# Optimization experiments

Measured on AMD Instinct MI355X. Metric: run time of the kernel, lower is better.

The kernel has to match this reference:

```python
import jax, jax.numpy as jnp
import numpy as np

HEADS = 16
NEG = -10000.0


def setup_inputs() -> dict:
    key = jax.random.key(0)
    ks = jax.random.split(key, 8)
    B, S, D = 2, 2048, 2048
    scale = 0.02
    return {
        "q": jax.random.normal(ks[0], (B, S, D), dtype=jnp.float32),
        "k": jax.random.normal(ks[1], (B, S, D), dtype=jnp.float32),
        "v": jax.random.normal(ks[2], (B, S, D), dtype=jnp.float32),
        "mask": jax.random.randint(ks[3], (B, S, S), 0, 2).astype(jnp.bool_),
        "Wq": jax.random.normal(ks[4], (D, D), dtype=jnp.float32) * scale,
        "Wk": jax.random.normal(ks[5], (D, D), dtype=jnp.float32) * scale,
        "Wv": jax.random.normal(ks[6], (D, D), dtype=jnp.float32) * scale,
        "Wo": jax.random.normal(ks[7], (D, D), dtype=jnp.float32) * scale,
    }


def _split_heads(x):
    # (B, S, D) -> (B, H, S, Dh)
    B, S, D = x.shape
    return x.reshape(B, S, HEADS, D // HEADS).transpose(0, 2, 1, 3)


def reference(q, k, v, mask, Wq, Wk, Wv, Wo):
    # bias-free linear projections (nn.Linear: x @ W.T)
    qp = q @ Wq.T
    kp = k @ Wk.T
    vp = v @ Wv.T
    qh, kh, vh = _split_heads(qp), _split_heads(kp), _split_heads(vp)
    head_dim = qh.shape[-1]
    # scores: (B, H, S, S)
    scores = jnp.einsum('bhqd,bhkd->bhqk', qh, kh) / jnp.sqrt(
        jnp.asarray(head_dim, dtype=qh.dtype))
    # additive mask, broadcast over heads (mask unsqueezed at -3 in torch)
    scores = scores + mask[:, None, :, :].astype(scores.dtype) * NEG
    attn = jax.nn.softmax(scores, axis=-1)
    ctx = jnp.einsum('bhqk,bhkd->bhqd', attn, vh)  # (B, H, S, Dh)
    B, H, S, Dh = ctx.shape
    ctx = ctx.transpose(0, 2, 1, 3).reshape(B, S, H * Dh)
    out = ctx @ Wo.T
    return (out, kp, vp)
```

## Files before the change

kernel.cpp:

```cpp
#include <hip/hip_runtime.h>
#include <hip/hip_bf16.h>
#include <stdint.h>


typedef unsigned short u16;
typedef unsigned char u8;
typedef __bf16 bf16x8 __attribute__((ext_vector_type(8)));
typedef unsigned short u16x8 __attribute__((ext_vector_type(8)));
typedef unsigned short u16x4 __attribute__((ext_vector_type(4)));
typedef float f32x4 __attribute__((ext_vector_type(4)));

#if __has_builtin(__builtin_amdgcn_exp2f)
#define EXP2(x) __builtin_amdgcn_exp2f(x)
#else
#define EXP2(x) exp2f(x)
#endif

__device__ __forceinline__ u16 f2bf(float f) {
  union { __bf16 h; u16 u; } c;
  c.h = (__bf16)f;
  return c.u;
}

__device__ __forceinline__ void stage8_f32(const float* src, u16* dst) {
  float4 x0 = ((const float4*)src)[0];
  float4 x1 = ((const float4*)src)[1];
  u16 t[8] = {f2bf(x0.x), f2bf(x0.y), f2bf(x0.z), f2bf(x0.w),
              f2bf(x1.x), f2bf(x1.y), f2bf(x1.z), f2bf(x1.w)};
  *(uint4*)dst = *(const uint4*)t;
}

typedef const __attribute__((address_space(1))) void gas_t;
typedef __attribute__((address_space(3))) void las_t;
__device__ __forceinline__ void gll16(const void* g, void* l) {
  __builtin_amdgcn_global_load_lds((gas_t*)g, (las_t*)l, 16, 0, 0);
}

__global__ void detect_kernel(const u16* __restrict__ q,
                              const u16* __restrict__ mask,
                              int* __restrict__ flags) {
  __shared__ int c32, oddnz, b3f80;
  if (threadIdx.x == 0) { c32 = 0; oddnz = 0; b3f80 = 0; }
  __syncthreads();
  int l32 = 0, lodd = 0, l3f = 0;
  for (int i = threadIdx.x; i < 4096; i += 256) {
    u16 u = q[i];
    if (((u >> 7) & 0xFF) >= 0x86) l32++;
    u16 m = mask[i];
    if (m == 0x3F80) l3f++;
    if ((i & 1) && m != 0) lodd++;
  }
  if (l32) atomicAdd(&c32, l32);
  if (lodd) atomicAdd(&oddnz, lodd);
  if (l3f) atomicAdd(&b3f80, l3f);
  __syncthreads();
  if (threadIdx.x == 0) {
    flags[0] = (c32 > 16) ? 1 : 0;
    flags[1] = b3f80 ? 2 : (oddnz ? 1 : 0);
  }
}

__global__ void pack_mask(const u8* __restrict__ maskp,
                          const int* __restrict__ flags,
                          u16* __restrict__ bits, long n) {
  const int mm = flags[1];
  long gw = ((long)blockIdx.x * blockDim.x + threadIdx.x) >> 6;
  int lane = threadIdx.x & 63;
  long nw = ((long)gridDim.x * blockDim.x) >> 6;
  for (long w = gw; w * 64 < n; w += nw) {
    long i = w * 64 + lane;
    bool nz;
    if (mm == 0)      nz = ((const int*)maskp)[i] != 0;
    else if (mm == 1) nz = maskp[i] != 0;
    else              nz = ((const u16*)maskp)[i] != 0;
    unsigned long long b = __ballot(nz);
    if (lane < 4) bits[w * 4 + lane] = (u16)(b >> (lane * 16));
  }
}

__global__ __launch_bounds__(256) void to_bf16_all(
    const u8* __restrict__ q, const u8* __restrict__ k, const u8* __restrict__ v,
    const u8* __restrict__ wq, const u8* __restrict__ wk,
    const u8* __restrict__ wv, const u8* __restrict__ wo,
    u16* __restrict__ qi, u16* __restrict__ ki, u16* __restrict__ vi,
    u16* __restrict__ wqb, u16* __restrict__ wkb, u16* __restrict__ wvb,
    u16* __restrict__ wob, const int* __restrict__ flags, long NEa, long NW) {
  const int fp = flags[0];
  const u8* src; u16* dst; long n;
  switch (blockIdx.y) {
    case 0: src = q;  dst = qi;  n = NEa; break;
    case 1: src = k;  dst = ki;  n = NEa; break;
    case 2: src = v;  dst = vi;  n = NEa; break;
    case 3: src = wq; dst = wqb; n = NW;  break;
    case 4: src = wk; dst = wkb; n = NW;  break;
    case 5: src = wv; dst = wvb; n = NW;  break;
    default: src = wo; dst = wob; n = NW; break;
  }
  long i0 = ((long)blockIdx.x * 256 + threadIdx.x) * 8;
  long stride = (long)gridDim.x * 256 * 8;
  for (long i = i0; i < n; i += stride) {
    u16 tmp[8];
    if (fp) stage8_f32((const float*)src + i, tmp);
    else    *(uint4*)tmp = *(const uint4*)((const u16*)src + i);
    *(uint4*)&dst[i] = *(const uint4*)tmp;
  }
}

__global__ __launch_bounds__(256) void transpose_v(
    const u8* __restrict__ vpbase, u16* __restrict__ vt,
    const int* __restrict__ flags, long NE, int B, int S, int H) {
  __shared__ u16 T[128 * 128];
  const int fp = flags[0];
  const int tid = threadIdx.x;
  const int s0 = blockIdx.x * 128, h = blockIdx.y, b = blockIdx.z;
  const int D = H * 128;
#pragma unroll
  for (int i = 0; i < 8; i++) {
    int t2 = i * 256 + tid;
    int si = t2 >> 4, cd = (t2 & 15) * 8;
    long off = (long)(b * S + s0 + si) * D + h * 128 + cd;
    u16 tmp[8];
    if (fp) stage8_f32((const float*)vpbase + 2 * NE + off, tmp);
    else    *(uint4*)tmp = *(const uint4*)((const u16*)vpbase + 2 * NE + off);
#pragma unroll
    for (int e = 0; e < 8; e++) {
      int d = cd + e;
      T[d * 128 + (si ^ (d & 15))] = tmp[e];
    }
  }
  __syncthreads();
#pragma unroll
  for (int i = 0; i < 8; i++) {
    int t2 = i * 256 + tid;
    int d = t2 >> 4, sc = (t2 & 15) * 8;
    u16 tmp[8];
#pragma unroll
    for (int e = 0; e < 8; e++)
      tmp[e] = T[d * 128 + ((sc + e) ^ (d & 15))];
    *(uint4*)&vt[((long)(b * H + h) * 128 + d) * S + s0 + sc] = *(const uint4*)tmp;
  }
}

#define BM 128
#define BN 128
#define BK 32

__device__ __forceinline__ void gemm_stage(
    const u8* __restrict__ Ab, const u8* __restrict__ Wbase,
    u16* __restrict__ AsD, u16* __restrict__ WsD,
    bool abf, bool wbf, int bm, int bn, int K, int k0, int tid, int wave) {
#pragma unroll
  for (int i = 0; i < 2; i++) {
    int t = i * 256 + tid;
    int r = t >> 2, c = (t & 3) * 8;
    long aoff = (long)(bm + r) * K + k0 + c;
    long woff = (long)(bn + r) * K + k0 + c;
    if (abf) gll16((const u16*)Ab + aoff, &AsD[(i * 256 + wave * 64) * 8]);
    else     stage8_f32((const float*)Ab + aoff, &AsD[t * 8]);
    if (wbf) gll16((const u16*)Wbase + woff, &WsD[(i * 256 + wave * 64) * 8]);
    else     stage8_f32((const float*)Wbase + woff, &WsD[t * 8]);
  }
}

__global__ __launch_bounds__(256) void gemm_xwT(
    const u8* __restrict__ Abase, const u8* __restrict__ Abase2,
    const u8* __restrict__ Abase3, const u8* __restrict__ Wbase,
    u8* __restrict__ Cbase, int c_slot, int amode, int qkv,
    const int* __restrict__ flags, int M, int N, int K,
    u16* __restrict__ dualbf) {
  __shared__ __align__(16) u16 As[3][BM * BK];
  __shared__ __align__(16) u16 Ws[3][BN * BK];
  const int fp = flags[0];
  const bool abf = (amode == 2) || (amode == 0) || !fp;
  const bool wbf = (amode == 2) || !fp;
  const bool pure = abf && wbf;
  const int tid = threadIdx.x;
  const int wave = tid >> 6, lane = tid & 63;
  const int lq = lane >> 4, lm = lane & 15;
  const int n = blockIdx.x;
  const int nbx = N >> 7;
  const int t3 = n >> 3;
  const int bx = t3 % nbx;
  const int by = (n & 7) + 8 * (t3 / nbx);
  const int bm = by * BM, bn = bx * BN;
  const int wm = (wave >> 1) * 64, wn = (wave & 1) * 64;
  const long MN = (long)M * N;
  const u8* Ab = Abase;
  if (qkv) {
    int blk = bn >> 11;
    Ab = (blk == 0) ? Abase : (blk == 1) ? Abase2 : Abase3;
  }
  f32x4 acc[4][4] = {};

  gemm_stage(Ab, Wbase, As[0], Ws[0], abf, wbf, bm, bn, K, 0, tid, wave);
  if (BK < K)
    gemm_stage(Ab, Wbase, As[1], Ws[1], abf, wbf, bm, bn, K, BK, tid, wave);

  int cur = 0;
  for (int k0 = 0; k0 < K; k0 += BK) {
    const bool more1 = (k0 + BK < K);
    const bool more2 = (k0 + 2 * BK < K);
    if (pure) {
      if (more1) asm volatile("s_waitcnt vmcnt(4)" ::: "memory");
      else       asm volatile("s_waitcnt vmcnt(0)" ::: "memory");
      __builtin_amdgcn_s_barrier();
    } else {
      __syncthreads();
    }
    if (more2) {
      int nxt = cur + 2; if (nxt >= 3) nxt -= 3;
      gemm_stage(Ab, Wbase, As[nxt], Ws[nxt], abf, wbf,
                 bm, bn, K, k0 + 2 * BK, tid, wave);
    }
    bf16x8 af[4], wf[4];
#pragma unroll
    for (int i = 0; i < 4; i++)
      af[i] = *(const bf16x8*)&As[cur][(wm + i * 16 + lm) * BK + lq * 8];
#pragma unroll
    for (int j = 0; j < 4; j++)
      wf[j] = *(const bf16x8*)&Ws[cur][(wn + j * 16 + lm) * BK + lq * 8];
#pragma unroll
    for (int i = 0; i < 4; i++)
#pragma unroll
      for (int j = 0; j < 4; j++)
        acc[i][j] = __builtin_amdgcn_mfma_f32_16x16x32_bf16(af[i], wf[j], acc[i][j], 0, 0, 0);
    cur += 1; if (cur >= 3) cur -= 3;
  }

  if (qkv) {
    const long NE2 = (long)M * 2048;
    const int blk = bn >> 11;
#pragma unroll
    for (int i = 0; i < 4; i++)
#pragma unroll
      for (int j = 0; j < 4; j++) {
        int col = bn + wn + j * 16 + lm;
        int lc = col & 2047;
#pragma unroll
        for (int r = 0; r < 4; r++) {
          int row = bm + wm + i * 16 + lq * 4 + r;
          long idx = (long)row * 2048 + lc;
          float v = acc[i][j][r];
          if (blk == 0) {
            ((u16*)Cbase)[idx] = f2bf(v);
          } else {
            if (fp) ((float*)Cbase)[(long)blk * NE2 + idx] = v;
            else    ((u16*)Cbase)[(long)blk * NE2 + idx] = f2bf(v);
            if (blk == 1) dualbf[idx] = f2bf(v);
          }
        }
      }
  } else {
#pragma unroll
    for (int i = 0; i < 4; i++)
#pragma unroll
      for (int j = 0; j < 4; j++)
#pragma unroll
        for (int r = 0; r < 4; r++) {
          int row = bm + wm + i * 16 + lq * 4 + r;
          int col = bn + wn + j * 16 + lm;
          long idx = (long)row * N + col;
          float v = acc[i][j][r];
          if (dualbf) dualbf[idx] = f2bf(v);
          if (c_slot < 0)  ((u16*)Cbase)[idx] = f2bf(v);
          else if (fp)     ((float*)Cbase)[(long)c_slot * MN + idx] = v;
          else             ((u16*)Cbase)[(long)c_slot * MN + idx] = f2bf(v);
        }
  }
}

#define AQ 128
#define AK 64
#define DH 128

__device__ __forceinline__ void attn_stageK(
    int kb, u16* __restrict__ KsD,
    const u16* __restrict__ kbf, const u8* __restrict__ kvbase,
    int use_kbf, int fp, long NE, int b, int h, int S, int D, int tid, int w) {
  const long kvoff = ((long)b * S + kb) * D + h * DH;
#pragma unroll
  for (int i = 0; i < 2; i++) {
    int t = i * 512 + tid;
    int r = t >> 4, c8 = t & 15;
    if (use_kbf) {
      gll16(kbf + kvoff + (long)r * D + (c8 ^ ((r & 3) << 2)) * 8,
            &KsD[(i * 512 + w * 64) * 8]);
    } else if (!fp) {
      gll16((const u16*)kvbase + NE + kvoff + (long)r * D + (c8 ^ ((r & 3) << 2)) * 8,
            &KsD[(i * 512 + w * 64) * 8]);
    } else {
      stage8_f32((const float*)kvbase + NE + kvoff + (long)r * D + (c8 ^ ((r & 3) << 2)) * 8,
                 &KsD[t * 8]);
    }
  }
}

__device__ __forceinline__ void attn_stageV(
    int kb, u16* __restrict__ VsD,
    const u8* __restrict__ kvbase, const u16* __restrict__ vtb,
    int use_vt, int fp, long NE, int b, int h, int S, int D, int tid, int w) {
  const long kvoff = ((long)b * S + kb) * D + h * DH;
#pragma unroll
  for (int i = 0; i < 2; i++) {
    int t = i * 512 + tid;
    int r = t >> 4, c8 = t & 15;
    if (use_vt) {
      int d = t >> 3, c = t & 7;
      gll16(vtb + (long)d * S + kb + ((c ^ (d & 7)) * 8),
            &VsD[(i * 512 + w * 64) * 8]);
    } else if (!fp) {
      gll16((const u16*)kvbase + 2 * NE + kvoff + (long)r * D + (c8 ^ (((r >> 3) & 3) << 1)) * 8,
            &VsD[(i * 512 + w * 64) * 8]);
    } else {
      stage8_f32((const float*)kvbase + 2 * NE + kvoff + (long)r * D + (c8 ^ (((r >> 3) & 3) << 1)) * 8,
                 &VsD[t * 8]);
    }
  }
}

__global__ __launch_bounds__(512) void attn_kernel(
    const u16* __restrict__ qp, const u8* __restrict__ kvbase,
    const u16* __restrict__ vt, const u16* __restrict__ kbf,
    const u8* __restrict__ maskp, const u16* __restrict__ bits,
    u16* __restrict__ ctx, const int* __restrict__ flags,
    int use_bits, int use_vt, int use_kbf, long NE, int B, int S, int H) {
  __shared__ __align__(16) u16 Ks[2][AK * DH];
  __shared__ __align__(16) u16 Vs[AK * DH];
  __shared__ __align__(16) u16 Ps[AQ * AK];
  const int fp = flags[0];
  const int mm = flags[1];
  const int tid = threadIdx.x;
  const int w = tid >> 6, lane = tid & 63;
  const int lq = lane >> 4, lm = lane & 15;
  const int nblk = blockIdx.x;
  const int q0 = ((nblk >> 3) & 15) * AQ;
  const int bh = (nblk >> 7) * 8 + (nblk & 7);
  const int h = bh & 15, b = bh >> 4;
  const int D = H * DH;
  const long qbase = ((long)b * S + q0) * D + h * DH;
  const u16* vtb = vt + (long)(b * H + h) * DH * S;
  const float C1 = 0.12751744f;
  const float CN = -28.8539008f;
  const float CM = -14455.8043f;
  const float CL = 86.5617f;

  bf16x8 qf[4];
#pragma unroll
  for (int ks = 0; ks < 4; ks++)
    qf[ks] = *(const bf16x8*)&qp[qbase + (long)(w * 16 + lm) * D + ks * 32 + lq * 8];

  float lrow[4] = {0.f, 0.f, 0.f, 0.f};
  f32x4 oacc[8] = {};

  attn_stageK(0, Ks[0], kbf, kvbase, use_kbf, fp, NE, b, h, S, D, tid, w);
  attn_stageV(0, Vs, kvbase, vtb, use_vt, fp, NE, b, h, S, D, tid, w);
  __syncthreads();

  int cur = 0;
  for (int kb = 0; kb < S; kb += AK) {
    const bool more = (kb + AK < S);
    u16x4 mbv[4];
    if (use_bits) {
#pragma unroll
      for (int r = 0; r < 4; r++) {
        int row = q0 + w * 16 + lq * 4 + r;
        mbv[r] = *(const u16x4*)&bits[(long)b * S * (S >> 4) + (long)row * (S >> 4) + (kb >> 4)];
      }
    }

    if (more)
      attn_stageK(kb + AK, Ks[cur ^ 1], kbf, kvbase, use_kbf, fp,
                  NE, b, h, S, D, tid, w);

    f32x4 sacc[4] = {};
#pragma unroll
    for (int ks = 0; ks < 4; ks++)
#pragma unroll
      for (int j = 0; j < 4; j++) {
        int krow = j * 16 + lm;
        int cc = (ks * 4 + lq) ^ ((lm & 3) << 2);
        bf16x8 kf = *(const bf16x8*)&Ks[cur][krow * DH + cc * 8];
        sacc[j] = __builtin_amdgcn_mfma_f32_16x16x32_bf16(qf[ks], kf, sacc[j], 0, 0, 0);
      }

#pragma unroll
    for (int j = 0; j < 4; j++)
#pragma unroll
      for (int r = 0; r < 4; r++) {
        bool mk;
        if (use_bits) {
          mk = (mbv[r][j] >> lm) & 1;
        } else {
          int row = q0 + w * 16 + lq * 4 + r;
          long midx = (long)b * S * S + (long)row * S + kb + j * 16 + lm;
          if (mm == 0)      mk = ((const int*)maskp)[midx] != 0;
          else if (mm == 1) mk = maskp[midx] != 0;
          else              mk = ((const u16*)maskp)[midx] != 0;
        }
        float arg = fmaf(sacc[j][r], C1, mk ? CM : CN);
        float p = EXP2(fminf(arg, CL));
        lrow[r] += p;
        Ps[(w * 16 + lq * 4 + r) * AK + ((j * 16 + lm) ^ (lq << 4))] = f2bf(p);
      }

    __syncthreads();

#pragma unroll
    for (int ks2 = 0; ks2 < 2; ks2++) {
      int prow = w * 16 + lm;
      int cb = (ks2 * 32 + lq * 8) ^ (((lm >> 2) & 3) << 4);
      bf16x8 pf = *(const bf16x8*)&Ps[prow * AK + cb];
      if (use_vt) {
#pragma unroll
        for (int tn = 0; tn < 8; tn++) {
          int d = tn * 16 + lm;
          int p = (ks2 * 4 + lq) ^ (lm & 7);
          bf16x8 vf = *(const bf16x8*)&Vs[d * 64 + p * 8];
          oacc[tn] = __builtin_amdgcn_mfma_f32_16x16x32_bf16(pf, vf, oacc[tn], 0, 0, 0);
        }
      } else {
#pragma unroll
        for (int tn = 0; tn < 8; tn++) {
          u16x8 vtmp;
#pragma unroll
          for (int jj = 0; jj < 8; jj++) {
            int s = ks2 * 32 + lq * 8 + jj;
            int d = (tn * 16 + lm) ^ (lq << 4);
            vtmp[jj] = Vs[s * DH + d];
          }
          bf16x8 vf = __builtin_bit_cast(bf16x8, vtmp);
          oacc[tn] = __builtin_amdgcn_mfma_f32_16x16x32_bf16(pf, vf, oacc[tn], 0, 0, 0);
        }
      }
    }

    __syncthreads();
    if (more)
      attn_stageV(kb + AK, Vs, kvbase, vtb, use_vt, fp,
                  NE, b, h, S, D, tid, w);
    cur ^= 1;
  }

  float linv[4];
#pragma unroll
  for (int r = 0; r < 4; r++) {
    float l = lrow[r];
#pragma unroll
    for (int o = 1; o < 16; o <<= 1) l += __shfl_xor(l, o);
    linv[r] = 1.f / fmaxf(l, 1e-30f);
  }
#pragma unroll
  for (int tn = 0; tn < 8; tn++)
#pragma unroll
    for (int r = 0; r < 4; r++) {
      int row = w * 16 + lq * 4 + r;
      int col = tn * 16 + lm;
      ctx[qbase + (long)row * D + col] = f2bf(oacc[tn][r] * linv[r]);
    }
}

extern "C" void kernel_launch(void* const* d_in, const int* in_sizes, int n_in,
                              void* d_out, int out_size, void* d_ws, size_t ws_size,
                              hipStream_t stream) {
  const int Bb = 2, S = 2048, Dm = 2048, H = 16;
  const int M = Bb * S;
  const long NE = (long)M * Dm;
  const long NEb = NE * 2;
  const long NW = (long)Dm * Dm;
  const long Wb = NW * 2;
  const long bits_bytes = (long)Bb * S * (S / 16) * 2;

  char* ws = (char*)d_ws;
  const size_t o_flags = (size_t)NEb;
  const size_t o_bits  = o_flags + 64;
  const size_t o_vt    = o_bits + (size_t)bits_bytes;
  const size_t o_kbf   = o_vt + (size_t)NEb;
  const size_t o_qi    = o_kbf + (size_t)NEb;
  const size_t o_ki    = o_qi + (size_t)NEb;
  const size_t o_vi    = o_ki + (size_t)NEb;
  const size_t o_wq    = o_vi + (size_t)NEb;
  const size_t o_wk    = o_wq + (size_t)Wb;
  const size_t o_wv    = o_wk + (size_t)Wb;
  const size_t o_wo    = o_wv + (size_t)Wb;
  const size_t o_end   = o_wo + (size_t)Wb;

  u16* qp    = (u16*)d_out;
  u16* ctx   = (u16*)ws;
  int* flags = (int*)(ws + o_flags);
  u16* bits  = (u16*)(ws + o_bits);
  u16* vt    = (u16*)(ws + o_vt);
  u16* kbf   = (u16*)(ws + o_kbf);
  u16* qi    = (u16*)(ws + o_qi);
  u16* ki    = (u16*)(ws + o_ki);
  u16* vi    = (u16*)(ws + o_vi);
  u16* wqb   = (u16*)(ws + o_wq);
  u16* wkb   = (u16*)(ws + o_wk);
  u16* wvb   = (u16*)(ws + o_wv);
  u16* wob   = (u16*)(ws + o_wo);

  const int use_bits = (ws_size >= o_vt)  ? 1 : 0;
  const int use_vt   = (ws_size >= o_kbf) ? 1 : 0;
  const int use_kbf  = (ws_size >= o_qi)  ? 1 : 0;
  const int use_conv = (ws_size >= o_end) ? 1 : 0;

  detect_kernel<<<1, 256, 0, stream>>>((const u16*)d_in[0], (const u16*)d_in[3], flags);
  if (use_bits)
    pack_mask<<<1024, 256, 0, stream>>>((const u8*)d_in[3], flags, bits, (long)Bb * S * S);

  dim3 gg(512);
  if (use_conv) {
    to_bf16_all<<<dim3(1024, 7), 256, 0, stream>>>(
        (const u8*)d_in[0], (const u8*)d_in[1], (const u8*)d_in[2],
        (const u8*)d_in[4], (const u8*)d_in[5], (const u8*)d_in[6], (const u8*)d_in[7],
        qi, ki, vi, wqb, wkb, wvb, wob, flags, NE, NW);
    gemm_xwT<<<dim3((M / 128) * (3 * Dm / 128)), 256, 0, stream>>>(
        (const u8*)qi, (const u8*)ki, (const u8*)vi, (const u8*)wqb,
        (u8*)d_out, 0, 2, 1, flags, M, 3 * Dm, Dm, kbf);
  } else {
    gemm_xwT<<<gg, 256, 0, stream>>>((const u8*)d_in[0], nullptr, nullptr,
                                     (const u8*)d_in[4],
                                     (u8*)qp, -1, 1, 0, flags, M, Dm, Dm, nullptr);
    gemm_xwT<<<gg, 256, 0, stream>>>((const u8*)d_in[1], nullptr, nullptr,
                                     (const u8*)d_in[5],
                                     (u8*)d_out, 1, 1, 0, flags, M, Dm, Dm,
                                     use_kbf ? kbf : nullptr);
    gemm_xwT<<<gg, 256, 0, stream>>>((const u8*)d_in[2], nullptr, nullptr,
                                     (const u8*)d_in[6],
                                     (u8*)d_out, 2, 1, 0, flags, M, Dm, Dm, nullptr);
  }
  if (use_vt)
    transpose_v<<<dim3(S / 128, H, Bb), 256, 0, stream>>>(
        (const u8*)d_out, vt, flags, NE, Bb, S, H);
  attn_kernel<<<dim3(512), 512, 0, stream>>>(
      qp, (const u8*)d_out, vt, kbf, (const u8*)d_in[3], bits, ctx, flags,
      use_bits, use_vt, use_kbf, NE, Bb, S, H);
  gemm_xwT<<<gg, 256, 0, stream>>>((const u8*)ctx, nullptr, nullptr,
                                   use_conv ? (const u8*)wob : (const u8*)d_in[7],
                                   (u8*)d_out, 0, use_conv ? 2 : 0, 0, flags, M, Dm, Dm, nullptr);
}
```

Before: 632.1 us.

## Prefetch K/V tiles through registers into single-buffered LDS

Replaces direct global-to-LDS async staging with double-buffered K by register prefetch of the next K and V tiles during compute, then writes them to single LDS buffers after the PV step. This removes the second K buffer, drops the mid-iteration barrier, and adds a launch bound hint for higher occupancy. Register pressure rises and may cause spills under the tighter occupancy bound, and the LDS write is now serialized behind compute.

```diff
diff --git a/kernel.cpp b/kernel.cpp
--- a/kernel.cpp
+++ b/kernel.cpp
@@ -273,58 +273,62 @@
 #define AK 64
 #define DH 128
 
-__device__ __forceinline__ void attn_stageK(
-    int kb, u16* __restrict__ KsD,
+__device__ __forceinline__ void attn_load(
+    int kb, uint4* kreg, uint4* vreg,
     const u16* __restrict__ kbf, const u8* __restrict__ kvbase,
-    int use_kbf, int fp, long NE, int b, int h, int S, int D, int tid, int w) {
+    const u16* __restrict__ vtb, int use_kbf, int use_vt, int fp,
+    long NE, int b, int h, int S, int D, int tid) {
   const long kvoff = ((long)b * S + kb) * D + h * DH;
 #pragma unroll
   for (int i = 0; i < 2; i++) {
     int t = i * 512 + tid;
     int r = t >> 4, c8 = t & 15;
     if (use_kbf) {
-      gll16(kbf + kvoff + (long)r * D + (c8 ^ ((r & 3) << 2)) * 8,
-            &KsD[(i * 512 + w * 64) * 8]);
+      kreg[i] = *(const uint4*)(kbf + kvoff + (long)r * D + c8 * 8);
     } else if (!fp) {
-      gll16((const u16*)kvbase + NE + kvoff + (long)r * D + (c8 ^ ((r & 3) << 2)) * 8,
-            &KsD[(i * 512 + w * 64) * 8]);
+      kreg[i] = *(const uint4*)((const u16*)kvbase + NE + kvoff + (long)r * D + c8 * 8);
     } else {
-      stage8_f32((const float*)kvbase + NE + kvoff + (long)r * D + (c8 ^ ((r & 3) << 2)) * 8,
-                 &KsD[t * 8]);
-    }
-  }
-}
-
-__device__ __forceinline__ void attn_stageV(
-    int kb, u16* __restrict__ VsD,
-    const u8* __restrict__ kvbase, const u16* __restrict__ vtb,
-    int use_vt, int fp, long NE, int b, int h, int S, int D, int tid, int w) {
-  const long kvoff = ((long)b * S + kb) * D + h * DH;
+      u16 tmp[8];
+      stage8_f32((const float*)kvbase + NE + kvoff + (long)r * D + c8 * 8, tmp);
+      kreg[i] = *(const uint4*)tmp;
+    }
+    if (use_vt) {
+      int d = t >> 3, c = t & 7;
+      vreg[i] = *(const uint4*)(vtb + (long)d * S + kb + c * 8);
+    } else if (!fp) {
+      vreg[i] = *(const uint4*)((const u16*)kvbase + 2 * NE + kvoff + (long)r * D + c8 * 8);
+    } else {
+      u16 tmp[8];
+      stage8_f32((const float*)kvbase + 2 * NE + kvoff + (long)r * D + c8 * 8, tmp);
+      vreg[i] = *(const uint4*)tmp;
+    }
+  }
+}
+
+__device__ __forceinline__ void attn_write(
+    const uint4* kreg, const uint4* vreg,
+    u16* __restrict__ Ks1, u16* __restrict__ Vs1, int use_vt, int tid) {
 #pragma unroll
   for (int i = 0; i < 2; i++) {
     int t = i * 512 + tid;
     int r = t >> 4, c8 = t & 15;
+    *(uint4*)&Ks1[(r * 16 + (c8 ^ ((r & 3) << 2))) * 8] = kreg[i];
     if (use_vt) {
       int d = t >> 3, c = t & 7;
-      gll16(vtb + (long)d * S + kb + ((c ^ (d & 7)) * 8),
-            &VsD[(i * 512 + w * 64) * 8]);
-    } else if (!fp) {
-      gll16((const u16*)kvbase + 2 * NE + kvoff + (long)r * D + (c8 ^ (((r >> 3) & 3) << 1)) * 8,
-            &VsD[(i * 512 + w * 64) * 8]);
+      *(uint4*)&Vs1[(d * 8 + (c ^ (d & 7))) * 8] = vreg[i];
     } else {
-      stage8_f32((const float*)kvbase + 2 * NE + kvoff + (long)r * D + (c8 ^ (((r >> 3) & 3) << 1)) * 8,
-                 &VsD[t * 8]);
-    }
-  }
-}
-
-__global__ __launch_bounds__(512) void attn_kernel(
+      *(uint4*)&Vs1[(r * 16 + (c8 ^ (((r >> 3) & 3) << 1))) * 8] = vreg[i];
+    }
+  }
+}
+
+__global__ __launch_bounds__(512, 4) void attn_kernel(
     const u16* __restrict__ qp, const u8* __restrict__ kvbase,
     const u16* __restrict__ vt, const u16* __restrict__ kbf,
     const u8* __restrict__ maskp, const u16* __restrict__ bits,
     u16* __restrict__ ctx, const int* __restrict__ flags,
     int use_bits, int use_vt, int use_kbf, long NE, int B, int S, int H) {
-  __shared__ __align__(16) u16 Ks[2][AK * DH];
+  __shared__ __align__(16) u16 Ks[AK * DH];
   __shared__ __align__(16) u16 Vs[AK * DH];
   __shared__ __align__(16) u16 Ps[AQ * AK];
   const int fp = flags[0];
@@ -351,12 +355,13 @@
 
   float lrow[4] = {0.f, 0.f, 0.f, 0.f};
   f32x4 oacc[8] = {};
-
-  attn_stageK(0, Ks[0], kbf, kvbase, use_kbf, fp, NE, b, h, S, D, tid, w);
-  attn_stageV(0, Vs, kvbase, vtb, use_vt, fp, NE, b, h, S, D, tid, w);
+  uint4 kreg[2], vreg[2];
+
+  attn_load(0, kreg, vreg, kbf, kvbase, vtb, use_kbf, use_vt, fp,
+            NE, b, h, S, D, tid);
+  attn_write(kreg, vreg, Ks, Vs, use_vt, tid);
   __syncthreads();
 
-  int cur = 0;
   for (int kb = 0; kb < S; kb += AK) {
     const bool more = (kb + AK < S);
     u16x4 mbv[4];
@@ -369,8 +374,8 @@
     }
 
     if (more)
-      attn_stageK(kb + AK, Ks[cur ^ 1], kbf, kvbase, use_kbf, fp,
-                  NE, b, h, S, D, tid, w);
+      attn_load(kb + AK, kreg, vreg, kbf, kvbase, vtb, use_kbf, use_vt, fp,
+                NE, b, h, S, D, tid);
 
     f32x4 sacc[4] = {};
 #pragma unroll
@@ -379,7 +384,7 @@
       for (int j = 0; j < 4; j++) {
         int krow = j * 16 + lm;
         int cc = (ks * 4 + lq) ^ ((lm & 3) << 2);
-        bf16x8 kf = *(const bf16x8*)&Ks[cur][krow * DH + cc * 8];
+        bf16x8 kf = *(const bf16x8*)&Ks[krow * DH + cc * 8];
         sacc[j] = __builtin_amdgcn_mfma_f32_16x16x32_bf16(qf[ks], kf, sacc[j], 0, 0, 0);
       }
 
@@ -403,8 +408,6 @@
         Ps[(w * 16 + lq * 4 + r) * AK + ((j * 16 + lm) ^ (lq << 4))] = f2bf(p);
       }
 
-    __syncthreads();
-
 #pragma unroll
     for (int ks2 = 0; ks2 < 2; ks2++) {
       int prow = w * 16 + lm;
@@ -435,10 +438,10 @@
     }
 
     __syncthreads();
-    if (more)
-      attn_stageV(kb + AK, Vs, kvbase, vtb, use_vt, fp,
-                  NE, b, h, S, D, tid, w);
-    cur ^= 1;
+    if (more) {
+      attn_write(kreg, vreg, Ks, Vs, use_vt, tid);
+    }
+    __syncthreads();
   }
 
   float linv[4];
```

Result: slower. 1.430 ms (+126.2%).
